# Kernel optimization log

Measured on AMD Instinct MI355X. Metric: run time of the kernel, lower is better.

## Reference

```python
import jax, jax.numpy as jnp
import numpy as np

EPS = 1e-5

def _bn(x, gamma, beta):
    # training-mode BatchNorm2d over (B, H, W) per channel, biased variance
    m = x.mean(axis=(0, 2, 3), keepdims=True)
    v = x.var(axis=(0, 2, 3), keepdims=True)
    return (x - m) * jax.lax.rsqrt(v + EPS) * gamma[None, :, None, None] + beta[None, :, None, None]

@jax.custom_vjp
def _atan_spike(x):
    # Heaviside forward, ATan surrogate (alpha=2) backward
    return (x >= 0.0).astype(x.dtype)

def _atan_fwd(x):
    return _atan_spike(x), x

def _atan_bwd(x, g):
    return (g / (1.0 + (jnp.pi * x) ** 2),)

_atan_spike.defvjp(_atan_fwd, _atan_bwd)

def setup_inputs() -> dict:
    key = jax.random.key(0)
    ks = jax.random.split(key, 3)
    T, N, Cin, Cout, H, W = 4, 8, 512, 256, 32, 32
    x = jax.random.normal(ks[0], (T, N, Cin, H, W), dtype=jnp.float32)
    bn1_gamma = jnp.ones((Cin,), jnp.float32)
    bn1_beta = jnp.zeros((Cin,), jnp.float32)
    conv_w = jax.random.normal(ks[1], (Cout, Cin, 1, 1), jnp.float32) / np.float32(np.sqrt(Cin))
    lif_w = jnp.zeros((1,), jnp.float32)  # sigmoid(0)=0.5 <=> init_tau=2.0
    bn2_gamma = jnp.ones((Cout,), jnp.float32)
    bn2_beta = jnp.zeros((Cout,), jnp.float32)
    up_w = jax.random.normal(ks[2], (Cout, Cout, 4, 4), jnp.float32) / np.float32(np.sqrt(Cout * 16))
    return {"x": x, "bn1_gamma": bn1_gamma, "bn1_beta": bn1_beta, "conv_w": conv_w,
            "lif_w": lif_w, "bn2_gamma": bn2_gamma, "bn2_beta": bn2_beta, "up_w": up_w}

def reference(x, bn1_gamma, bn1_beta, conv_w, lif_w, bn2_gamma, bn2_beta, up_w):
    T, N, Cin, H, W = x.shape
    Cout = conv_w.shape[0]
    # bottleneck: SeqToANNContainer(BN(Cin), Conv2d 1x1 Cin->Cout, no bias)
    xf = x.reshape(T * N, Cin, H, W)
    h = _bn(xf, bn1_gamma, bn1_beta)
    h = jnp.einsum('bchw,oc->bohw', h, conv_w[:, :, 0, 0])
    h = h.reshape(T, N, Cout, H, W)
    # MultiStepParametricLIFNode: v += (x - v)*sigmoid(w); hard reset to 0, detach_reset
    tau_inv = jax.nn.sigmoid(lif_w[0])
    def step(v, xt):
        v = v + (xt - v) * tau_inv
        s = _atan_spike(v - 1.0)
        v = v * (1.0 - jax.lax.stop_gradient(s))
        return v, s
    _, spikes = jax.lax.scan(step, jnp.zeros_like(h[0]), h)
    s = spikes.reshape(T * N, Cout, H, W)
    # ConstantDilation2d(dilation=2): zero-insertion -> (2H-1, 2W-1)
    d = jnp.zeros((T * N, Cout, 2 * H - 1, 2 * W - 1), s.dtype).at[:, :, ::2, ::2].set(s)
    # ConstantPad2d(kernel-1-padding = 4-1-1 = 2)
    d = jnp.pad(d, ((0, 0), (0, 0), (2, 2), (2, 2)))
    d = _bn(d, bn2_gamma, bn2_beta)
    # ConvTranspose2d(k=4, stride=1, padding=3) == VALID conv with channel-swapped, flipped kernel
    kern = up_w.transpose(1, 0, 2, 3)[:, :, ::-1, ::-1]
    out = jax.lax.conv_general_dilated(d, kern, (1, 1), 'VALID',
                                       dimension_numbers=('NCHW', 'OIHW', 'NCHW'))
    return out.reshape(T, N, Cout, 2 * H, 2 * W)
```

## Files before the change

### kernel.cpp

```cpp
#include <hip/hip_runtime.h>
#include <math.h>

#define CIN 512
#define COUT 256
#define TT 4
#define NN 8
#define HH 32
#define WW 32
#define FR (TT*NN)
#define HW (HH*WW)
#define BN_EPS 1e-5
#define FLAGCAP (1<<20)
#define N2 143648.0

typedef unsigned short ushort_t;
typedef unsigned int uint_t;
typedef __attribute__((ext_vector_type(8))) short short8;
typedef __attribute__((ext_vector_type(4))) float f32x4;
typedef __attribute__((ext_vector_type(4))) uint_t u32x4;

__device__ inline ushort_t f2bf(float f) {
    uint_t u = __float_as_uint(f);
    uint_t r = u + 0x7FFFu + ((u >> 16) & 1u);
    return (ushort_t)(r >> 16);
}
__device__ inline float bf2f(ushort_t a) { return __uint_as_float(((uint_t)a) << 16); }

__global__ __launch_bounds__(256) void k_bn1_stats(const float* __restrict__ x,
                                                   const float* __restrict__ gamma1,
                                                   double* __restrict__ mean,
                                                   double* __restrict__ alpha) {
    int c = blockIdx.x;
    int tid = threadIdx.x;
    double s1 = 0.0, s2 = 0.0;
    const float4* x4 = reinterpret_cast<const float4*>(x);
    for (int f = 0; f < FR; ++f) {
        size_t base4 = ((size_t)(f * CIN + c) * HW) >> 2;
        float4 v = x4[base4 + tid];
        s1 += (double)v.x + (double)v.y + (double)v.z + (double)v.w;
        s2 += (double)v.x * v.x + (double)v.y * v.y + (double)v.z * v.z + (double)v.w * v.w;
    }
    __shared__ double l1[256], l2[256];
    l1[tid] = s1; l2[tid] = s2;
    __syncthreads();
    for (int ofs = 128; ofs > 0; ofs >>= 1) {
        if (tid < ofs) { l1[tid] += l1[tid + ofs]; l2[tid] += l2[tid + ofs]; }
        __syncthreads();
    }
    if (tid == 0) {
        double n = (double)(FR * HW);
        double m = l1[0] / n;
        double var = l2[0] / n - m * m;
        mean[c] = m;
        alpha[c] = (double)gamma1[c] / sqrt(var + BN_EPS);
    }
}

__global__ __launch_bounds__(256) void k_xsplit(const float* __restrict__ x,
                                                ushort_t* __restrict__ Xa_g,
                                                ushort_t* __restrict__ Xb_g,
                                                float* __restrict__ X2_g) {
    int blk = blockIdx.x;
    int n = blk >> 6;
    int hw0 = (blk & 63) << 4;
    int tid = threadIdx.x;
    int pg = tid & 3;
    int rr = tid >> 2;

    __shared__ ushort_t La[8192];
    __shared__ ushort_t Lb[8192];
    __shared__ float X2s[64];

    float x2loc[16];
#pragma unroll
    for (int q = 0; q < 16; ++q) x2loc[q] = 0.f;
    if (tid < 64) X2s[tid] = 0.f;

    for (int kc = 0; kc < 4; ++kc) {
        int c0 = kc << 7;
        __syncthreads();
#pragma unroll
        for (int sw = 0; sw < 8; ++sw) {
            const int t = sw >> 1;
            int i = ((sw & 1) << 6) + rr;
            const float4 v = *reinterpret_cast<const float4*>(
                &x[(((size_t)((t * NN + n) * CIN) + c0 + i) << 10) + hw0 + (pg << 2)]);
            int cbl = i >> 3, e = i & 7;
#pragma unroll
            for (int k = 0; k < 4; ++k) {
                float xv = (k == 0) ? v.x : (k == 1) ? v.y : (k == 2) ? v.z : v.w;
                ushort_t a = f2bf(xv);
                ushort_t b = f2bf(xv - bf2f(a));
                x2loc[(k << 2) + t] += xv * xv;
                int lrx = (k << 2) + t;
                uint_t u = ((((uint_t)(pg * 16 + cbl)) * 16 + lrx) << 3) + e;
                uint_t byteoff = (u << 1) ^ ((uint_t)pg << 5);
                *(ushort_t*)((char*)La + byteoff) = a;
                *(ushort_t*)((char*)Lb + byteoff) = b;
            }
        }
        __syncthreads();
        for (int q = tid; q < 1024; q += 256) {
            int pg2 = q >> 8;
            uint_t lo = (uint_t)(q & 255) << 4;
            uint_t src = (((uint_t)pg2 << 12) + lo) ^ ((uint_t)pg2 << 5);
            u32x4 va = *(u32x4*)((char*)La + src);
            u32x4 vb = *(u32x4*)((char*)Lb + src);
            size_t dst = (((size_t)blk * 4 + pg2) << 13) + ((size_t)kc << 11) + ((size_t)(q & 255) << 3);
            __builtin_nontemporal_store(va, (u32x4*)(Xa_g + dst));
            __builtin_nontemporal_store(vb, (u32x4*)(Xb_g + dst));
        }
    }
    __syncthreads();
#pragma unroll
    for (int k = 0; k < 4; ++k)
#pragma unroll
        for (int t = 0; t < 4; ++t)
            atomicAdd(&X2s[pg * 16 + k * 4 + t], x2loc[(k << 2) + t]);
    __syncthreads();
    if (tid < 64) X2_g[(blk << 6) + tid] = X2s[tid];
}

__global__ __launch_bounds__(256) void k_prep_wsplit(const float* __restrict__ conv_w,
                                                     const float* __restrict__ beta1,
                                                     const double* __restrict__ mean,
                                                     const double* __restrict__ alpha,
                                                     double* __restrict__ w2t,
                                                     ushort_t* __restrict__ Wa,
                                                     ushort_t* __restrict__ Wb,
                                                     float* __restrict__ W2,
                                                     double* __restrict__ bias) {
    int o = blockIdx.x;
    float s2 = 0.f;
    double sb = 0.0;
    for (int c = threadIdx.x; c < CIN; c += 256) {
        double cw = (double)conv_w[(size_t)o * CIN + c];
        double w = cw * alpha[c];
        w2t[(size_t)c * COUT + o] = w;
        float wf = (float)w;
        ushort_t a = f2bf(wf);
        ushort_t b = f2bf(wf - bf2f(a));
        size_t base = ((size_t)(c >> 3) * COUT + o) * 8 + (c & 7);
        Wa[base] = a; Wb[base] = b;
        s2 += wf * wf;
        sb += ((double)beta1[c] - mean[c] * alpha[c]) * cw;
    }
    __shared__ float red[256];
    __shared__ double redd[256];
    red[threadIdx.x] = s2;
    redd[threadIdx.x] = sb;
    __syncthreads();
    for (int ofs = 128; ofs > 0; ofs >>= 1) {
        if (threadIdx.x < ofs) {
            red[threadIdx.x] += red[threadIdx.x + ofs];
            redd[threadIdx.x] += redd[threadIdx.x + ofs];
        }
        __syncthreads();
    }
    if (threadIdx.x == 0) { W2[o] = red[0]; bias[o] = redd[0]; }
}

__global__ __launch_bounds__(256) void k_gemm_lif_mfma(
    const ushort_t* __restrict__ Xa_g, const ushort_t* __restrict__ Xb_g,
    const ushort_t* __restrict__ Wa, const ushort_t* __restrict__ Wb,
    const float* __restrict__ X2_g, const float* __restrict__ W2,
    const double* __restrict__ bias, const float* __restrict__ lif_w,
    ushort_t* __restrict__ spk, int* __restrict__ cnt,
    uint_t* __restrict__ flags, uint_t* __restrict__ flagcnt)
{
    int blk = blockIdx.x;
    int n   = blk >> 6;
    int hw0 = (blk & 63) << 4;
    int tid = threadIdx.x;
    int wv = tid >> 6, lane = tid & 63;
    int lr = lane & 15, kq = lane >> 4;
    int pxh = wv >> 1, oh = wv & 1;

    __shared__ uint_t cl[4 * 64 * 8];

    f32x4 acc[2][8];
#pragma unroll
    for (int m = 0; m < 2; ++m)
#pragma unroll
        for (int ot = 0; ot < 8; ++ot) acc[m][ot] = (f32x4){0.f, 0.f, 0.f, 0.f};

    const ushort_t* xa0 = Xa_g + (((size_t)blk) << 15) + ((size_t)pxh << 14) + ((uint_t)lane << 3);
    const ushort_t* xb0 = Xb_g + (((size_t)blk) << 15) + ((size_t)pxh << 14) + ((uint_t)lane << 3);
    const ushort_t* wbase_a = Wa + ((uint_t)kq << 11) + ((uint_t)oh << 10) + ((uint_t)lr << 3);
    const ushort_t* wbase_b = Wb + ((uint_t)kq << 11) + ((uint_t)oh << 10) + ((uint_t)lr << 3);

#pragma unroll 2
    for (int ks = 0; ks < 16; ++ks) {
        short8 fa0 = *(const short8*)(xa0 + (ks << 9));
        short8 fa1 = *(const short8*)(xa0 + 8192 + (ks << 9));
        short8 fb0 = *(const short8*)(xb0 + (ks << 9));
        short8 fb1 = *(const short8*)(xb0 + 8192 + (ks << 9));
        const ushort_t* wpa = wbase_a + (ks << 13);
        const ushort_t* wpb = wbase_b + (ks << 13);
#pragma unroll
        for (int ot = 0; ot < 8; ++ot) {
            short8 wa8 = *(const short8*)(wpa + (ot << 7));
            short8 wb8 = *(const short8*)(wpb + (ot << 7));
            acc[0][ot] = __builtin_amdgcn_mfma_f32_16x16x32_bf16(fa0, wa8, acc[0][ot], 0, 0, 0);
            acc[1][ot] = __builtin_amdgcn_mfma_f32_16x16x32_bf16(fa1, wa8, acc[1][ot], 0, 0, 0);
            acc[0][ot] = __builtin_amdgcn_mfma_f32_16x16x32_bf16(fb0, wa8, acc[0][ot], 0, 0, 0);
            acc[1][ot] = __builtin_amdgcn_mfma_f32_16x16x32_bf16(fb1, wa8, acc[1][ot], 0, 0, 0);
            acc[0][ot] = __builtin_amdgcn_mfma_f32_16x16x32_bf16(fa0, wb8, acc[0][ot], 0, 0, 0);
            acc[1][ot] = __builtin_amdgcn_mfma_f32_16x16x32_bf16(fa1, wb8, acc[1][ot], 0, 0, 0);
        }
    }

    float xs2[2][4];
#pragma unroll
    for (int m = 0; m < 2; ++m)
#pragma unroll
        for (int t = 0; t < 4; ++t)
            xs2[m][t] = X2_g[(blk << 6) + (((pxh << 1) + m) << 4) + (kq << 2) + t];

    for (int q = tid; q < 4 * 64 * 8; q += 256) cl[q] = 0;
    __syncthreads();

    double tau = 1.0 / (1.0 + exp(-(double)lif_w[0]));
#pragma unroll
    for (int ot = 0; ot < 8; ++ot) {
        int o = (oh << 7) + (ot << 4) + lr;
        double bi = bias[o];
        float w2v = W2[o];
        uint_t cloc = 0;
#pragma unroll
        for (int m = 0; m < 2; ++m) {
            int hw = hw0 + (pxh << 3) + (m << 2) + kq;
            double v = 0.0;
            bool fl = false;
#pragma unroll
            for (int t = 0; t < 4; ++t) {
                double h = (double)acc[m][ot][t] + bi;
                double eps = (double)(4e-5f * sqrtf(w2v * xs2[m][t]) + 1e-6f);
                v += (h - v) * tau;
                if (fabs(v - 1.0) <= 2.0 * eps) fl = true;
                bool s = (v >= 1.0);
                spk[((size_t)((t * NN + n) * HW) + hw) * COUT + o] = s ? (ushort_t)0x3F80 : (ushort_t)0;
                cloc += s ? 1u : 0u;
                if (s) v = 0.0;
            }
            if (fl) {
                uint_t id = atomicAdd(flagcnt, 1u);
                if (id < FLAGCAP) flags[id] = (((uint_t)(n * HW + hw)) << 8) | (uint_t)o;
            }
        }
        cl[(wv << 9) + (lane << 3) + ot] = cloc;
    }
    __syncthreads();
    {
        int o = tid;
        int ohh = o >> 7, ott = (o >> 4) & 7, lr2 = o & 15;
        uint_t s = 0;
#pragma unroll
        for (int w2 = ohh; w2 < 4; w2 += 2)
#pragma unroll
            for (int k2 = 0; k2 < 4; ++k2)
                s += cl[(w2 << 9) + (((k2 << 4) + lr2) << 3) + ott];
        if (s) atomicAdd(&cnt[o], (int)s);
    }
}

__global__ __launch_bounds__(256) void k_fixup(
    const float* __restrict__ x, const double* __restrict__ w2t,
    const double* __restrict__ bias, const float* __restrict__ lif_w,
    const uint_t* __restrict__ flags, const uint_t* __restrict__ flagcnt,
    ushort_t* __restrict__ spk, int* __restrict__ cnt)
{
    int nf = (int)*flagcnt; if (nf > FLAGCAP) nf = FLAGCAP;
    int wid = (blockIdx.x << 2) + (threadIdx.x >> 6);
    int lane = threadIdx.x & 63;
    double tau = 1.0 / (1.0 + exp(-(double)lif_w[0]));
    for (int g = wid; g < nf; g += 1024) {
        uint_t f = flags[g];
        int o = f & 255;
        int s = f >> 8;
        int n = s >> 10, hw = s & 1023;
        double h[4];
#pragma unroll
        for (int t = 0; t < 4; ++t) {
            double p = 0.0;
            for (int c = lane; c < CIN; c += 64)
                p += w2t[(size_t)c * COUT + o] *
                     (double)x[(((size_t)((t * NN + n) * CIN) + c) << 10) + hw];
#pragma unroll
            for (int ofs = 32; ofs > 0; ofs >>= 1) p += __shfl_down(p, ofs);
            h[t] = p;
        }
        if (lane == 0) {
            double bi = bias[o];
            double v = 0.0; int delta = 0;
#pragma unroll
            for (int t = 0; t < 4; ++t) {
                v += (h[t] + bi - v) * tau;
                bool sn = (v >= 1.0);
                size_t idx = ((size_t)((t * NN + n) * HW) + hw) * COUT + o;
                ushort_t old = spk[idx];
                ushort_t nw = sn ? (ushort_t)0x3F80 : (ushort_t)0;
                if (old != nw) { spk[idx] = nw; delta += sn ? 1 : -1; }
                if (sn) v = 0.0;
            }
            if (delta) atomicAdd(&cnt[o], delta);
        }
    }
}

__global__ __launch_bounds__(256) void k_wt_prep(const float* __restrict__ up_w,
                                                 const int* __restrict__ cnt,
                                                 const float* __restrict__ gamma2,
                                                 ushort_t* __restrict__ Wt) {
    int blk = blockIdx.x;
    int ij = blk >> 5, cb = blk & 31;
    int o = threadIdx.x;
    __shared__ double a2s[8];
    if (o < 8) {
        int c = (cb << 3) + o;
        double m = (double)cnt[c] / N2;
        a2s[o] = (double)gamma2[c] / sqrt(m - m * m + BN_EPS);
    }
    __syncthreads();
    short8 v;
#pragma unroll
    for (int e = 0; e < 8; ++e) {
        int c = (cb << 3) + e;
        float w = (float)(a2s[e] * (double)up_w[(((size_t)c * COUT) + o) * 16 + ij]);
        v[e] = (short)f2bf(w);
    }
    *(short8*)(Wt + ((size_t)ij << 16) + ((size_t)cb << 11) + ((size_t)o << 3)) = v;
}

__global__ __launch_bounds__(256) void k_kconst(const float* __restrict__ up_w,
                                                const int* __restrict__ cnt,
                                                const float* __restrict__ gamma2,
                                                const float* __restrict__ beta2,
                                                float* __restrict__ kc) {
    int o = blockIdx.x, c = threadIdx.x;
    double m = (double)cnt[c] / N2;
    double a = (double)gamma2[c] / sqrt(m - m * m + BN_EPS);
    double b2v = (double)beta2[c] - m * a;
    const float* u = up_w + ((size_t)c * COUT + o) * 16;
    double t = 0.0;
#pragma unroll
    for (int k = 0; k < 16; ++k) t += (double)u[k];
    double s = b2v * t;
    __shared__ double red[256];
    red[c] = s;
    __syncthreads();
    for (int ofs = 128; ofs > 0; ofs >>= 1) {
        if (c < ofs) red[c] += red[c + ofs];
        __syncthreads();
    }
    if (c == 0) kc[o] = (float)red[0];
}

__global__ __launch_bounds__(512) void k_deconv_mfma(const ushort_t* __restrict__ spk,
                                                     const ushort_t* __restrict__ Wt,
                                                     const float* __restrict__ kc,
                                                     float* __restrict__ out) {
    int p = blockIdx.x;
    int w = ((p & 7) << 7) + (p >> 3);
    int b  = w >> 5;
    int py = (w >> 4) & 1;
    int Yb = (w & 15) << 1;
    int tid = threadIdx.x;
    int wv  = tid >> 6;
    int lane = tid & 63;
    int px = wv >> 2;
    int og = wv & 3;
    int lr = lane & 15;
    int kq = lane >> 4;

    __shared__ __align__(16) char smem[52224];
    ushort_t* slab = (ushort_t*)smem;

    int sb = Yb - 1 + py;
    for (int q = tid; q < 3 * 34 * 32; q += 512) {
        int pix = q >> 5;
        int l = q & 31;
        int r = pix / 34;
        int xc = pix - r * 34;
        int sy = sb + r;
        int sx = xc - 1;
        uint_t off = ((uint_t)(pix << 9) + (uint_t)(l << 4)) ^ ((uint_t)(xc & 7) << 4);
        uint4* dst = (uint4*)((char*)slab + off);
        if (sy >= 0 && sy < 32 && sx >= 0 && sx < 32) {
            *dst = *(const uint4*)(spk + ((size_t)b * HW + sy * 32 + sx) * COUT + l * 8);
        } else {
            *dst = make_uint4(0u, 0u, 0u, 0u);
        }
    }
    __syncthreads();

    f32x4 acc[4][4];
#pragma unroll
    for (int pf = 0; pf < 4; ++pf)
#pragma unroll
        for (int of = 0; of < 4; ++of)
            acc[pf][of] = (f32x4){0.f, 0.f, 0.f, 0.f};

    int obase = og << 6;

#pragma unroll
    for (int dy = 0; dy < 2; ++dy) {
#pragma unroll
        for (int dx = 0; dx < 2; ++dx) {
            int i = 3 - py - 2 * dy;
            int j = 3 - px - 2 * dx;
            const ushort_t* wpij = Wt + ((size_t)(i * 4 + j) << 16);
            uint_t sbase[4], swz[4];
#pragma unroll
            for (int pf = 0; pf < 4; ++pf) {
                int pid = pf * 16 + lr;
                int Yq = pid >> 5;
                int X  = pid & 31;
                int xc = X + dx + px;
                int prow = (Yq + dy) * 34 + xc;
                sbase[pf] = ((uint_t)prow << 9) + ((uint_t)kq << 4);
                swz[pf]   = ((uint_t)(xc & 7)) << 4;
            }
#pragma unroll
            for (int cs = 0; cs < 8; ++cs) {
                short8 aw[4];
#pragma unroll
                for (int of = 0; of < 4; ++of)
                    aw[of] = *(const short8*)(wpij +
                        ((size_t)((cs << 2) + kq) * COUT + obase + (of << 4) + lr) * 8);
                short8 bs[4];
#pragma unroll
                for (int pf = 0; pf < 4; ++pf)
                    bs[pf] = *(const short8*)((const char*)slab +
                              ((sbase[pf] + ((uint_t)cs << 6)) ^ swz[pf]));
#pragma unroll
                for (int pf = 0; pf < 4; ++pf)
#pragma unroll
                    for (int of = 0; of < 4; ++of)
                        acc[pf][of] = __builtin_amdgcn_mfma_f32_16x16x32_bf16(
                            aw[of], bs[pf], acc[pf][of], 0, 0, 0);
            }
        }
    }

    __syncthreads();
    float* stage = (float*)smem;
#pragma unroll 1
    for (int of = 0; of < 4; ++of) {
        if (of) __syncthreads();
#pragma unroll
        for (int rg = 0; rg < 4; ++rg) {
            int row = (og << 4) + (kq << 2) + rg;
#pragma unroll
            for (int pf = 0; pf < 4; ++pf) {
                int Yq = pf >> 1;
                int x = ((((pf & 1) << 4) + lr) << 1) + px;
                uint_t a4 = ((uint_t)row << 5) + ((uint_t)Yq << 4)
                          + (((uint_t)x >> 2) ^ ((uint_t)kq << 2));
                stage[(a4 << 2) + (x & 3)] = acc[pf][of][rg];
            }
        }
        __syncthreads();
#pragma unroll
        for (int rep = 0; rep < 4; ++rep) {
            int u = tid + (rep << 9);
            int r = u >> 5, rem = u & 31;
            int yq = rem >> 4, f4 = rem & 15;
            uint_t a4 = ((uint_t)r << 5) + ((uint_t)yq << 4)
                      + ((uint_t)f4 ^ ((((uint_t)r >> 2) & 3) << 2));
            f32x4 v = ((const f32x4*)stage)[a4];
            int o = ((r >> 4) << 6) + (of << 4) + (r & 15);
            float base = kc[o];
            v[0] += base; v[1] += base; v[2] += base; v[3] += base;
            int y = ((Yb + yq) << 1) + py;
            __builtin_nontemporal_store(v,
                (f32x4*)(out + ((size_t)(b * COUT + o) << 12) + (y << 6) + (f4 << 2)));
        }
    }
}

extern "C" void kernel_launch(void* const* d_in, const int* in_sizes, int n_in,
                              void* d_out, int out_size, void* d_ws, size_t ws_size,
                              hipStream_t stream) {
    (void)in_sizes; (void)n_in; (void)out_size; (void)ws_size;
    const float* x        = (const float*)d_in[0];
    const float* bn1_g    = (const float*)d_in[1];
    const float* bn1_b    = (const float*)d_in[2];
    const float* conv_w   = (const float*)d_in[3];
    const float* lif_w    = (const float*)d_in[4];
    const float* bn2_g    = (const float*)d_in[5];
    const float* bn2_b    = (const float*)d_in[6];
    const float* up_w     = (const float*)d_in[7];
    float* out = (float*)d_out;

    char* ws = (char*)d_ws;
    ushort_t* spk  = (ushort_t*)(ws + 0);
    ushort_t* Xa_g = (ushort_t*)(ws + 16777216);
    ushort_t* Xb_g = (ushort_t*)(ws + 50331648);
    float*  X2_g   = (float*)  (ws + 83886080);
    float*  W2     = (float*)  (ws + 84017152);
    double* mean   = (double*) (ws + 84018176);
    double* alpha  = (double*) (ws + 84022272);
    double* w2t    = (double*) (ws + 84026368);
    double* bias   = (double*) (ws + 85074944);
    int*    cnt    = (int*)    (ws + 85081088);
    float*  kc     = (float*)  (ws + 85082112);
    ushort_t* Wt   = (ushort_t*)(ws + 85083136);
    ushort_t* Wa   = (ushort_t*)(ws + 87180288);
    ushort_t* Wb   = (ushort_t*)(ws + 87442432);
    uint_t* flagcnt= (uint_t*) (ws + 87704576);
    uint_t* flags  = (uint_t*) (ws + 87705600);

    hipMemsetAsync(cnt, 0, COUT * sizeof(int), stream);
    hipMemsetAsync(flagcnt, 0, sizeof(uint_t), stream);

    k_bn1_stats<<<CIN, 256, 0, stream>>>(x, bn1_g, mean, alpha);
    k_xsplit<<<512, 256, 0, stream>>>(x, Xa_g, Xb_g, X2_g);
    k_prep_wsplit<<<COUT, 256, 0, stream>>>(conv_w, bn1_b, mean, alpha, w2t, Wa, Wb, W2, bias);
    k_gemm_lif_mfma<<<512, 256, 0, stream>>>(Xa_g, Xb_g, Wa, Wb, X2_g, W2,
                                             bias, lif_w, spk, cnt, flags, flagcnt);
    k_fixup<<<256, 256, 0, stream>>>(x, w2t, bias, lif_w, flags, flagcnt, spk, cnt);
    k_wt_prep<<<512, 256, 0, stream>>>(up_w, cnt, bn2_g, Wt);
    k_kconst<<<COUT, 256, 0, stream>>>(up_w, cnt, bn2_g, bn2_b, kc);
    k_deconv_mfma<<<32 * 2 * 16, 512, 0, stream>>>(spk, Wt, kc, out);
}
```

Measured before the change: 417.5 us.

## Fuse BN1 statistics into xsplit pass and load deconv spikes directly from global

Removes the separate BN1 statistics kernel, which re-read the full input, and accumulates per-channel sums inside the xsplit pass using wave shuffles and double atomics, followed by a tiny finalize kernel. The deconv kernel drops its LDS slab staging and instead loads spike vectors straight from global memory with bounds masks, relying on cache reuse. This saves one full read of x and a barrier, but the partial sums are now accumulated in float before the double atomics, and the direct global loads in the MFMA loop may add latency. FLAGCAP is also halved.

```diff
diff --git a/kernel.cpp b/kernel.cpp
--- a/kernel.cpp
+++ b/kernel.cpp
@@ -10,7 +10,7 @@
 #define FR (TT*NN)
 #define HW (HH*WW)
 #define BN_EPS 1e-5
-#define FLAGCAP (1<<20)
+#define FLAGCAP (1<<19)
 #define N2 143648.0
 
 typedef unsigned short ushort_t;
@@ -26,40 +26,12 @@
 }
 __device__ inline float bf2f(ushort_t a) { return __uint_as_float(((uint_t)a) << 16); }
 
-__global__ __launch_bounds__(256) void k_bn1_stats(const float* __restrict__ x,
-                                                   const float* __restrict__ gamma1,
-                                                   double* __restrict__ mean,
-                                                   double* __restrict__ alpha) {
-    int c = blockIdx.x;
-    int tid = threadIdx.x;
-    double s1 = 0.0, s2 = 0.0;
-    const float4* x4 = reinterpret_cast<const float4*>(x);
-    for (int f = 0; f < FR; ++f) {
-        size_t base4 = ((size_t)(f * CIN + c) * HW) >> 2;
-        float4 v = x4[base4 + tid];
-        s1 += (double)v.x + (double)v.y + (double)v.z + (double)v.w;
-        s2 += (double)v.x * v.x + (double)v.y * v.y + (double)v.z * v.z + (double)v.w * v.w;
-    }
-    __shared__ double l1[256], l2[256];
-    l1[tid] = s1; l2[tid] = s2;
-    __syncthreads();
-    for (int ofs = 128; ofs > 0; ofs >>= 1) {
-        if (tid < ofs) { l1[tid] += l1[tid + ofs]; l2[tid] += l2[tid + ofs]; }
-        __syncthreads();
-    }
-    if (tid == 0) {
-        double n = (double)(FR * HW);
-        double m = l1[0] / n;
-        double var = l2[0] / n - m * m;
-        mean[c] = m;
-        alpha[c] = (double)gamma1[c] / sqrt(var + BN_EPS);
-    }
-}
-
 __global__ __launch_bounds__(256) void k_xsplit(const float* __restrict__ x,
                                                 ushort_t* __restrict__ Xa_g,
                                                 ushort_t* __restrict__ Xb_g,
-                                                float* __restrict__ X2_g) {
+                                                float* __restrict__ X2_g,
+                                                double* __restrict__ bn_s1,
+                                                double* __restrict__ bn_s2) {
     int blk = blockIdx.x;
     int n = blk >> 6;
     int hw0 = (blk & 63) << 4;
@@ -72,10 +44,14 @@
     __shared__ float X2s[64];
 
     float x2loc[16];
+    float s1v[8], s2v[8];
 #pragma unroll
     for (int q = 0; q < 16; ++q) x2loc[q] = 0.f;
+#pragma unroll
+    for (int q = 0; q < 8; ++q) { s1v[q] = 0.f; s2v[q] = 0.f; }
     if (tid < 64) X2s[tid] = 0.f;
 
+#pragma unroll
     for (int kc = 0; kc < 4; ++kc) {
         int c0 = kc << 7;
         __syncthreads();
@@ -86,12 +62,15 @@
             const float4 v = *reinterpret_cast<const float4*>(
                 &x[(((size_t)((t * NN + n) * CIN) + c0 + i) << 10) + hw0 + (pg << 2)]);
             int cbl = i >> 3, e = i & 7;
+            int slot = (kc << 1) + (sw & 1);
 #pragma unroll
             for (int k = 0; k < 4; ++k) {
                 float xv = (k == 0) ? v.x : (k == 1) ? v.y : (k == 2) ? v.z : v.w;
                 ushort_t a = f2bf(xv);
                 ushort_t b = f2bf(xv - bf2f(a));
                 x2loc[(k << 2) + t] += xv * xv;
+                s1v[slot] += xv;
+                s2v[slot] += xv * xv;
                 int lrx = (k << 2) + t;
                 uint_t u = ((((uint_t)(pg * 16 + cbl)) * 16 + lrx) << 3) + e;
                 uint_t byteoff = (u << 1) ^ ((uint_t)pg << 5);
@@ -111,6 +90,17 @@
             __builtin_nontemporal_store(vb, (u32x4*)(Xb_g + dst));
         }
     }
+#pragma unroll
+    for (int slot = 0; slot < 8; ++slot) {
+        float a1 = s1v[slot], a2v = s2v[slot];
+        a1 += __shfl_xor(a1, 1); a1 += __shfl_xor(a1, 2);
+        a2v += __shfl_xor(a2v, 1); a2v += __shfl_xor(a2v, 2);
+        if (pg == 0) {
+            int c = ((slot >> 1) << 7) + ((slot & 1) << 6) + rr;
+            atomicAdd(&bn_s1[c], (double)a1);
+            atomicAdd(&bn_s2[c], (double)a2v);
+        }
+    }
     __syncthreads();
 #pragma unroll
     for (int k = 0; k < 4; ++k)
@@ -119,6 +109,19 @@
             atomicAdd(&X2s[pg * 16 + k * 4 + t], x2loc[(k << 2) + t]);
     __syncthreads();
     if (tid < 64) X2_g[(blk << 6) + tid] = X2s[tid];
+}
+
+__global__ __launch_bounds__(512) void k_bn1_fin(const double* __restrict__ bn_s1,
+                                                 const double* __restrict__ bn_s2,
+                                                 const float* __restrict__ gamma1,
+                                                 double* __restrict__ mean,
+                                                 double* __restrict__ alpha) {
+    int c = threadIdx.x;
+    double n = (double)(FR * HW);
+    double m = bn_s1[c] / n;
+    double var = bn_s2[c] / n - m * m;
+    mean[c] = m;
+    alpha[c] = (double)gamma1[c] / sqrt(var + BN_EPS);
 }
 
 __global__ __launch_bounds__(256) void k_prep_wsplit(const float* __restrict__ conv_w,
@@ -373,26 +376,7 @@
     int lr = lane & 15;
     int kq = lane >> 4;
 
-    __shared__ __align__(16) char smem[52224];
-    ushort_t* slab = (ushort_t*)smem;
-
-    int sb = Yb - 1 + py;
-    for (int q = tid; q < 3 * 34 * 32; q += 512) {
-        int pix = q >> 5;
-        int l = q & 31;
-        int r = pix / 34;
-        int xc = pix - r * 34;
-        int sy = sb + r;
-        int sx = xc - 1;
-        uint_t off = ((uint_t)(pix << 9) + (uint_t)(l << 4)) ^ ((uint_t)(xc & 7) << 4);
-        uint4* dst = (uint4*)((char*)slab + off);
-        if (sy >= 0 && sy < 32 && sx >= 0 && sx < 32) {
-            *dst = *(const uint4*)(spk + ((size_t)b * HW + sy * 32 + sx) * COUT + l * 8);
-        } else {
-            *dst = make_uint4(0u, 0u, 0u, 0u);
-        }
-    }
-    __syncthreads();
+    __shared__ __align__(16) float stage[8192];
 
     f32x4 acc[4][4];
 #pragma unroll
@@ -402,6 +386,7 @@
             acc[pf][of] = (f32x4){0.f, 0.f, 0.f, 0.f};
 
     int obase = og << 6;
+    const short8 ZV = {0,0,0,0,0,0,0,0};
 
 #pragma unroll
     for (int dy = 0; dy < 2; ++dy) {
@@ -410,16 +395,19 @@
             int i = 3 - py - 2 * dy;
             int j = 3 - px - 2 * dx;
             const ushort_t* wpij = Wt + ((size_t)(i * 4 + j) << 16);
-            uint_t sbase[4], swz[4];
+            const ushort_t* pptr[4];
+            bool okv[4];
 #pragma unroll
             for (int pf = 0; pf < 4; ++pf) {
-                int pid = pf * 16 + lr;
+                int pid = (pf << 4) + lr;
                 int Yq = pid >> 5;
                 int X  = pid & 31;
-                int xc = X + dx + px;
-                int prow = (Yq + dy) * 34 + xc;
-                sbase[pf] = ((uint_t)prow << 9) + ((uint_t)kq << 4);
-                swz[pf]   = ((uint_t)(xc & 7)) << 4;
+                int sy = Yb + Yq + dy + py - 1;
+                int sx = X + dx + px - 1;
+                bool ok = (sy >= 0) && (sy < 32) && (sx >= 0) && (sx < 32);
+                int pix = ok ? ((b << 10) + (sy << 5) + sx) : 0;
+                okv[pf] = ok;
+                pptr[pf] = spk + (((size_t)pix) << 8) + (kq << 3);
             }
 #pragma unroll
             for (int cs = 0; cs < 8; ++cs) {
@@ -431,8 +419,7 @@
                 short8 bs[4];
 #pragma unroll
                 for (int pf = 0; pf < 4; ++pf)
-                    bs[pf] = *(const short8*)((const char*)slab +
-                              ((sbase[pf] + ((uint_t)cs << 6)) ^ swz[pf]));
+                    bs[pf] = okv[pf] ? *(const short8*)(pptr[pf] + (cs << 5)) : ZV;
 #pragma unroll
                 for (int pf = 0; pf < 4; ++pf)
 #pragma unroll
@@ -443,8 +430,6 @@
         }
     }
 
-    __syncthreads();
-    float* stage = (float*)smem;
 #pragma unroll 1
     for (int of = 0; of < 4; ++of) {
         if (of) __syncthreads();
@@ -510,12 +495,15 @@
     ushort_t* Wb   = (ushort_t*)(ws + 87442432);
     uint_t* flagcnt= (uint_t*) (ws + 87704576);
     uint_t* flags  = (uint_t*) (ws + 87705600);
+    double* bn_s1  = (double*) (ws + 89802752);
+    double* bn_s2  = (double*) (ws + 89806848);
 
     hipMemsetAsync(cnt, 0, COUT * sizeof(int), stream);
     hipMemsetAsync(flagcnt, 0, sizeof(uint_t), stream);
-
-    k_bn1_stats<<<CIN, 256, 0, stream>>>(x, bn1_g, mean, alpha);
-    k_xsplit<<<512, 256, 0, stream>>>(x, Xa_g, Xb_g, X2_g);
+    hipMemsetAsync(bn_s1, 0, 2 * CIN * sizeof(double), stream);
+
+    k_xsplit<<<512, 256, 0, stream>>>(x, Xa_g, Xb_g, X2_g, bn_s1, bn_s2);
+    k_bn1_fin<<<1, 512, 0, stream>>>(bn_s1, bn_s2, bn1_g, mean, alpha);
     k_prep_wsplit<<<COUT, 256, 0, stream>>>(conv_w, bn1_b, mean, alpha, w2t, Wa, Wb, W2, bias);
     k_gemm_lif_mfma<<<512, 256, 0, stream>>>(Xa_g, Xb_g, Wa, Wb, X2_g, W2,
                                              bias, lif_w, spk, cnt, flags, flagcnt);
```

Measured after the change: 610.2 us. 1.46x slower.
